# Optimization experiments

Measured on AMD Instinct MI355X. Metric: run time of the kernel, lower is better.

## Reference

```python
import jax, jax.numpy as jnp
import numpy as np

KERNEL = 3          # route_nms_kernel
MAX_ROUTES = 256    # max_routes (topk per image)
STRIDE = 4.0        # route_stride
MIN_SIZE = 32.0     # route_min_size
MAX_SIZE = 512.0    # route_max_size
POWER = 2.0         # route_score_power
B, H, W = 32, 512, 512


def setup_inputs() -> dict:
    key = jax.random.key(0)
    k1, k2, k3 = jax.random.split(key, 3)
    return {
        "route_logits": jax.random.normal(k1, (B, 1, H, W), dtype=jnp.float32),
        "scale_logits": jax.random.normal(k2, (B, 1, H, W), dtype=jnp.float32),
        "uncertainty_logits": jax.random.normal(k3, (B, 1, H, W), dtype=jnp.float32),
        "image_h": 2048,
        "image_w": 2048,
    }


def _local_max_pool(x):
    # x: [H, W]; 3x3 max pool, stride 1, pad kernel//2 (torch F.max_pool2d pads with -inf)
    pad = KERNEL // 2
    return jax.lax.reduce_window(x, -jnp.inf, jax.lax.max,
                                 (KERNEL, KERNEL), (1, 1),
                                 [(pad, pad), (pad, pad)])


def reference(route_logits, scale_logits, uncertainty_logits, image_h, image_w):
    # score_map = sigmoid(logits)^power * (1 - 0.35*sigmoid(uncertainty))  (use_route_uncertainty=True)
    score_map = jnp.power(jax.nn.sigmoid(route_logits), POWER)
    score_map = score_map * (1.0 - 0.35 * jax.nn.sigmoid(uncertainty_logits))
    img_h = jnp.float32(image_h)
    img_w = jnp.float32(image_w)
    width = route_logits.shape[-1]

    def per_image(batch_idx, scores2d, scale2d, unc2d):
        pooled = _local_max_pool(scores2d)
        filtered = jnp.where(scores2d == pooled, scores2d, -1.0)  # masked_fill(~mask, -1)
        values, indices = jax.lax.top_k(filtered.reshape(-1), MAX_ROUTES)
        valid = values > 0.0  # torch filters values>0; here kept as fixed-shape mask
        ys = indices // width
        xs = indices % width
        cx = (xs.astype(jnp.float32) + 0.5) * STRIDE
        cy = (ys.astype(jnp.float32) + 0.5) * STRIDE
        scale_g = scale2d[ys, xs]
        unc = jax.nn.sigmoid(unc2d[ys, xs])
        side = MIN_SIZE + jax.nn.sigmoid(scale_g) * (MAX_SIZE - MIN_SIZE)
        side = side * (1.0 + 0.25 * unc)
        half = side * 0.5
        x1 = jnp.clip(cx - half, 0.0, img_w - 1.0)
        y1 = jnp.clip(cy - half, 0.0, img_h - 1.0)
        x2 = jnp.clip(cx + half, 1.0, img_w)
        y2 = jnp.clip(cy + half, 1.0, img_h)
        rois = jnp.stack([jnp.full_like(x1, batch_idx), x1, y1, x2, y2], axis=1)  # [K,5]
        rois = jnp.where(valid[:, None], rois, 0.0)
        vals = jnp.where(valid, values, 0.0)
        return rois, vals, valid

    batch_ids = jnp.arange(route_logits.shape[0], dtype=jnp.float32)
    rois, scores, valid = jax.vmap(per_image)(
        batch_ids, score_map[:, 0], scale_logits[:, 0], uncertainty_logits[:, 0])
    # rois: [B, K, 5], scores: [B, K], valid: [B, K] (per_image_counts = valid.sum(-1))
    return rois, scores, valid
```

## Files before the change

kernel.cpp:

```cpp
#include <hip/hip_runtime.h>
#include <cstdint>
#include <cstddef>

#define BATCH 32
#define IMH 512
#define IMW 512
#define KMAX 256

#define RPW 4
#define NBLKX 2
#define NYG (IMH / RPW)
#define NL1 (NBLKX * NYG)
#define NM1 (NL1 / 4)
#define WCAP 256

typedef unsigned long long u64;

__device__ __forceinline__ float sigmoidf_(float x) {
    return 1.0f / (1.0f + expf(-x));
}
__device__ __forceinline__ float scoref_(float r, float u) {
    const float sg = sigmoidf_(r);
    return sg * sg * (1.0f - 0.35f * sigmoidf_(u));
}

#define SHF(v, jj, dm) do {                                         \
    const u64 o_ = __shfl_xor((v), (jj), 64);                       \
    const bool take_ = ((((lane & (jj)) == 0) == (dm)) == ((v) < o_)); \
    (v) = take_ ? o_ : (v);                                         \
} while (0)

#define RMAX(a, b) do {                                             \
    const u64 hi_ = ((a) > (b)) ? (a) : (b);                        \
    const u64 lo_ = ((a) > (b)) ? (b) : (a);                        \
    (a) = hi_; (b) = lo_;                                           \
} while (0)

#define RMIN(a, b) do {                                             \
    const u64 hi_ = ((a) > (b)) ? (a) : (b);                        \
    const u64 lo_ = ((a) > (b)) ? (b) : (a);                        \
    (a) = lo_; (b) = hi_;                                           \
} while (0)

__device__ __forceinline__ void clean256(u64& v0, u64& v1, u64& v2, u64& v3,
                                         const int lane) {
    RMAX(v0, v2); RMAX(v1, v3);
    RMAX(v0, v1); RMAX(v2, v3);
    #pragma unroll
    for (int j = 32; j > 0; j >>= 1) {
        SHF(v0, j, true); SHF(v1, j, true); SHF(v2, j, true); SHF(v3, j, true);
    }
}

__device__ __forceinline__ void sort256(u64& v0, u64& v1, u64& v2, u64& v3,
                                        const int lane) {
    #pragma unroll
    for (int k = 2; k <= 32; k <<= 1) {
        #pragma unroll
        for (int j = k >> 1; j > 0; j >>= 1) {
            const bool dm = ((lane & k) == 0);
            SHF(v0, j, dm); SHF(v1, j, dm); SHF(v2, j, dm); SHF(v3, j, dm);
        }
    }
    #pragma unroll
    for (int j = 32; j > 0; j >>= 1) {
        SHF(v0, j, true); SHF(v1, j, false); SHF(v2, j, true); SHF(v3, j, false);
    }
    RMAX(v0, v1); RMIN(v2, v3);
    #pragma unroll
    for (int j = 32; j > 0; j >>= 1) {
        SHF(v0, j, true); SHF(v1, j, true); SHF(v2, j, false); SHF(v3, j, false);
    }
    clean256(v0, v1, v2, v3, lane);
}

__device__ __forceinline__ void sort128(u64& v0, u64& v1, const int lane) {
    #pragma unroll
    for (int k = 2; k <= 32; k <<= 1) {
        #pragma unroll
        for (int j = k >> 1; j > 0; j >>= 1) {
            const bool dm = ((lane & k) == 0);
            SHF(v0, j, dm); SHF(v1, j, dm);
        }
    }
    #pragma unroll
    for (int j = 32; j > 0; j >>= 1) {
        SHF(v0, j, true); SHF(v1, j, false);
    }
    RMAX(v0, v1);
    #pragma unroll
    for (int j = 32; j > 0; j >>= 1) {
        SHF(v0, j, true); SHF(v1, j, true);
    }
}

__device__ __forceinline__ void merge256(u64& v0, u64& v1, u64& v2, u64& v3,
                                         u64 w0, u64 w1, u64 w2, u64 w3,
                                         const int lane) {
    const int rl = 63 ^ lane;
    const u64 b0 = __shfl(w3, rl, 64);
    const u64 b1 = __shfl(w2, rl, 64);
    const u64 b2 = __shfl(w1, rl, 64);
    const u64 b3 = __shfl(w0, rl, 64);
    v0 = (v0 > b0) ? v0 : b0;
    v1 = (v1 > b1) ? v1 : b1;
    v2 = (v2 > b2) ? v2 : b2;
    v3 = (v3 > b3) ? v3 : b3;
    clean256(v0, v1, v2, v3, lane);
}

__device__ __forceinline__ void load256(const u64* p, u64& v0, u64& v1,
                                        u64& v2, u64& v3, const int lane) {
    v0 = p[lane]; v1 = p[lane + 64]; v2 = p[lane + 128]; v3 = p[lane + 192];
}
__device__ __forceinline__ void store256(u64* p, u64 v0, u64 v1,
                                         u64 v2, u64 v3, const int lane) {
    p[lane] = v0; p[lane + 64] = v1; p[lane + 128] = v2; p[lane + 192] = v3;
}

__device__ __forceinline__ void merge4s(const u64* p,
                                        u64& a0, u64& a1, u64& a2, u64& a3,
                                        const int lane) {
    load256(p, a0, a1, a2, a3, lane);
    u64 w0, w1, w2, w3;
    load256(p + KMAX, w0, w1, w2, w3, lane);
    merge256(a0, a1, a2, a3, w0, w1, w2, w3, lane);
    u64 c0, c1, c2, c3;
    load256(p + 2 * KMAX, c0, c1, c2, c3, lane);
    load256(p + 3 * KMAX, w0, w1, w2, w3, lane);
    merge256(c0, c1, c2, c3, w0, w1, w2, w3, lane);
    merge256(a0, a1, a2, a3, c0, c1, c2, c3, lane);
}

__global__ __launch_bounds__(128)
void score_nms_kernel(const float* __restrict__ route,
                      const float* __restrict__ unc,
                      u64* __restrict__ top) {
    const int b    = blockIdx.z;
    const int w    = threadIdx.x >> 6;
    const int lane = threadIdx.x & 63;
    const int yg   = blockIdx.y * 2 + w;
    const int y0   = yg * RPW;
    const int x0   = blockIdx.x * 256 + lane * 4;
    const int list = yg * NBLKX + blockIdx.x;

    __shared__ u64 lcand[2 * WCAP];
    u64* myR = lcand + w * WCAP;

    const float* rB = route + (size_t)b * IMH * IMW;
    const float* uB = unc   + (size_t)b * IMH * IMW;

    int ex = -1;
    if (lane == 0)       ex = x0 - 1;
    else if (lane == 63) ex = x0 + 4;
    const bool eAct = (ex >= 0 && ex < IMW);

    const u64 laneMaskLt = (1ull << lane) - 1ull;
    int wcnt = 0;

    float sP[4], hP1[4], hP2[4];
    #pragma unroll
    for (int j = 0; j < 4; ++j) { sP[j] = -INFINITY; hP1[j] = -INFINITY; hP2[j] = -INFINITY; }

    const int ylast = y0 + RPW;
    bool v = (y0 - 1 >= 0);
    float4 r4, u4; float er = 0.f, eu = 0.f;
    if (v) {
        r4 = *(const float4*)(rB + (size_t)(y0 - 1) * IMW + x0);
        u4 = *(const float4*)(uB + (size_t)(y0 - 1) * IMW + x0);
        if (eAct) { er = rB[(size_t)(y0 - 1) * IMW + ex]; eu = uB[(size_t)(y0 - 1) * IMW + ex]; }
    }

    for (int y = y0 - 1; y <= ylast; ++y) {
        const int yn = y + 1;
        const bool vn = (yn <= ylast) && (yn < IMH);
        float4 r4n, u4n; float ern = 0.f, eun = 0.f;
        if (vn) {
            r4n = *(const float4*)(rB + (size_t)yn * IMW + x0);
            u4n = *(const float4*)(uB + (size_t)yn * IMW + x0);
            if (eAct) { ern = rB[(size_t)yn * IMW + ex]; eun = uB[(size_t)yn * IMW + ex]; }
        }

        float sC[4], hmC[4];
        float es = -INFINITY;
        if (v && eAct) es = scoref_(er, eu);
        if (v) {
            sC[0] = scoref_(r4.x, u4.x);
            sC[1] = scoref_(r4.y, u4.y);
            sC[2] = scoref_(r4.z, u4.z);
            sC[3] = scoref_(r4.w, u4.w);
        } else {
            sC[0] = sC[1] = sC[2] = sC[3] = -INFINITY;
        }
        float lft = __shfl_up(sC[3], 1, 64);
        if (lane == 0) lft = es;
        float rgt = __shfl_down(sC[0], 1, 64);
        if (lane == 63) rgt = es;
        if (v) {
            hmC[0] = fmaxf(fmaxf(lft,   sC[0]), sC[1]);
            hmC[1] = fmaxf(fmaxf(sC[0], sC[1]), sC[2]);
            hmC[2] = fmaxf(fmaxf(sC[1], sC[2]), sC[3]);
            hmC[3] = fmaxf(fmaxf(sC[2], sC[3]), rgt);
        } else {
            hmC[0] = hmC[1] = hmC[2] = hmC[3] = -INFINITY;
        }

        if (y >= y0 + 1) {
            const int yo = y - 1;
            bool p[4]; int cntT = 0;
            #pragma unroll
            for (int j = 0; j < 4; ++j) {
                const float m9 = fmaxf(fmaxf(hP2[j], hP1[j]), hmC[j]);
                p[j] = (sP[j] >= m9);
                cntT += p[j] ? 1 : 0;
            }
            const u64 B0 = __ballot(cntT & 1);
            const u64 B1 = __ballot(cntT & 2);
            const u64 B2 = __ballot(cntT & 4);
            const int total = __popcll(B0) + 2 * __popcll(B1) + 4 * __popcll(B2);
            if (total > 0) {
                const int prefix = __popcll(B0 & laneMaskLt) + 2 * __popcll(B1 & laneMaskLt)
                                 + 4 * __popcll(B2 & laneMaskLt);
                int mb = wcnt + prefix;
                #pragma unroll
                for (int j = 0; j < 4; ++j) {
                    if (p[j]) {
                        const unsigned idx = (unsigned)(yo * IMW + (x0 + j));
                        const u64 key = ((u64)__float_as_uint(sP[j]) << 32) | (unsigned)(~idx);
                        if (mb < WCAP) myR[mb] = key;
                        ++mb;
                    }
                }
                wcnt += total;
            }
        }

        #pragma unroll
        for (int j = 0; j < 4; ++j) { hP2[j] = hP1[j]; hP1[j] = hmC[j]; sP[j] = sC[j]; }
        r4 = r4n; u4 = u4n; er = ern; eu = eun; v = vn;
    }

    const int m = (wcnt < WCAP) ? wcnt : WCAP;
    u64 a0, a1, a2, a3;
    if (m <= 128) {
        a0 = (lane      < m) ? myR[lane]      : 0ull;
        a1 = (lane + 64 < m) ? myR[lane + 64] : 0ull;
        sort128(a0, a1, lane);
        a2 = 0ull; a3 = 0ull;
    } else {
        a0 = (lane       < m) ? myR[lane]       : 0ull;
        a1 = (lane + 64  < m) ? myR[lane + 64]  : 0ull;
        a2 = (lane + 128 < m) ? myR[lane + 128] : 0ull;
        a3 = (lane + 192 < m) ? myR[lane + 192] : 0ull;
        sort256(a0, a1, a2, a3, lane);
    }

    u64* seg = top + ((size_t)b * NL1 + list) * KMAX;
    store256(seg, a0, a1, a2, a3, lane);
}

__global__ __launch_bounds__(128)
void merge4_kernel(const u64* __restrict__ in, int nin,
                   u64* __restrict__ out_) {
    const int w    = threadIdx.x >> 6;
    const int lane = threadIdx.x & 63;
    const int o    = blockIdx.x * 2 + w;
    const int b    = blockIdx.y;
    const int nout = nin / 4;
    if (o >= nout) return;

    const u64* L = in + ((size_t)b * nin + o * 4) * KMAX;
    u64 a0, a1, a2, a3;
    merge4s(L, a0, a1, a2, a3, lane);

    u64* out = out_ + ((size_t)b * nout + o) * KMAX;
    store256(out, a0, a1, a2, a3, lane);
}

__global__ __launch_bounds__(1024)
void fused_tail_kernel(const u64* __restrict__ mid,
                       const float* __restrict__ scale,
                       const float* __restrict__ unc,
                       const int* __restrict__ imh,
                       const int* __restrict__ imw,
                       float* __restrict__ rois,
                       float* __restrict__ scoresOut,
                       float* __restrict__ validOut) {
    const int b    = blockIdx.x;
    const int tid  = threadIdx.x;
    const int w    = tid >> 6;
    const int lane = tid & 63;

    __shared__ u64 bufA[16 * KMAX];
    __shared__ u64 bufB[8 * KMAX];

    {
        const u64* G = mid + ((size_t)b * NM1 + 4 * w) * KMAX;
        u64 a0, a1, a2, a3;
        merge4s(G, a0, a1, a2, a3, lane);
        store256(bufA + (size_t)w * KMAX, a0, a1, a2, a3, lane);
    }
    __syncthreads();

    u64* src = bufA;
    u64* dst = bufB;
    int nl = 16;
    while (nl > 1) {
        const int half = nl >> 1;
        const int E = half * KMAX;
        for (int p = tid; p < E; p += 1024) {
            const int h = p >> 8;
            const int i = p & (KMAX - 1);
            const u64 a = src[(2 * h) * KMAX + i];
            const u64 c = src[(2 * h + 1) * KMAX + (KMAX - 1 - i)];
            dst[p] = (a > c) ? a : c;
        }
        __syncthreads();
        for (int j = KMAX >> 1; j > 0; j >>= 1) {
            for (int p = tid; p < (E >> 1); p += 1024) {
                const int i   = ((p & ~(j - 1)) << 1) | (p & (j - 1));
                const int ixj = i | j;
                const u64 a = dst[i];
                const u64 c = dst[ixj];
                if (a < c) { dst[i] = c; dst[ixj] = a; }
            }
            __syncthreads();
        }
        u64* t = src; src = dst; dst = t;
        nl = half;
    }

    if (tid < KMAX) {
        const u64 k = src[tid];
        const float value = __uint_as_float((unsigned)(k >> 32));
        const bool valid  = (k != 0ull) && (value > 0.0f);

        float r0 = 0.f, r1 = 0.f, r2 = 0.f, r3 = 0.f, r4 = 0.f, sv = 0.f, vv = 0.f;
        if (valid) {
            const unsigned idx = ~(unsigned)(k & 0xFFFFFFFFull);
            const int y = (int)(idx / IMW);
            const int x = (int)(idx % IMW);
            const float cx = ((float)x + 0.5f) * 4.0f;
            const float cy = ((float)y + 0.5f) * 4.0f;
            const float sg = scale[(size_t)b * IMH * IMW + idx];
            const float uu = unc[(size_t)b * IMH * IMW + idx];
            const float su = sigmoidf_(uu);
            float side = 32.0f + sigmoidf_(sg) * (512.0f - 32.0f);
            side = side * (1.0f + 0.25f * su);
            const float half2 = side * 0.5f;
            const float fw = (float)imw[0];
            const float fh = (float)imh[0];
            r0 = (float)b;
            r1 = fminf(fmaxf(cx - half2, 0.0f), fw - 1.0f);
            r2 = fminf(fmaxf(cy - half2, 0.0f), fh - 1.0f);
            r3 = fminf(fmaxf(cx + half2, 1.0f), fw);
            r4 = fminf(fmaxf(cy + half2, 1.0f), fh);
            sv = value;
            vv = 1.0f;
        }
        float* roiP = rois + ((size_t)b * KMAX + tid) * 5;
        roiP[0] = r0; roiP[1] = r1; roiP[2] = r2; roiP[3] = r3; roiP[4] = r4;
        scoresOut[b * KMAX + tid] = sv;
        validOut[b * KMAX + tid]  = vv;
    }
}

extern "C" void kernel_launch(void* const* d_in, const int* in_sizes, int n_in,
                              void* d_out, int out_size, void* d_ws, size_t ws_size,
                              hipStream_t stream) {
    const float* route = (const float*)d_in[0];
    const float* scale = (const float*)d_in[1];
    const float* unc   = (const float*)d_in[2];
    const int*   imh   = (const int*)d_in[3];
    const int*   imw   = (const int*)d_in[4];

    u64* top  = (u64*)d_ws;
    u64* mid1 = top + (size_t)BATCH * NL1 * KMAX;

    float* rois      = (float*)d_out;
    float* scoresOut = rois + (size_t)BATCH * KMAX * 5;
    float* validOut  = scoresOut + (size_t)BATCH * KMAX;

    dim3 grid1(NBLKX, NYG / 2, BATCH);
    score_nms_kernel<<<grid1, 128, 0, stream>>>(route, unc, top);

    dim3 grid2(NM1 / 2, BATCH);
    merge4_kernel<<<grid2, 128, 0, stream>>>(top, NL1, mid1);

    fused_tail_kernel<<<BATCH, 1024, 0, stream>>>(mid1, scale, unc, imh, imw,
                                                  rois, scoresOut, validOut);
}
```

Measured before the change: 62.72 us.

## Split score computation into separate pass and add extra merge stage before tail

Score computation moves out of the NMS kernel into a standalone elementwise kernel that writes a score map to workspace, which the NMS kernel then reads. This avoids recomputing sigmoids for halo rows and edge pixels and halves the loads per pixel inside the NMS kernel. The fused tail's first merge level becomes a separate merge4 launch, and the tail runs on 512 threads using a plain copy into shared memory. In exchange, a 32 MB score map is written and read back through global memory and two extra kernel launches are added.

```diff
diff --git a/kernel.cpp b/kernel.cpp
--- a/kernel.cpp
+++ b/kernel.cpp
@@ -12,7 +12,10 @@
 #define NYG (IMH / RPW)
 #define NL1 (NBLKX * NYG)
 #define NM1 (NL1 / 4)
+#define NMID (NM1 / 4)
 #define WCAP 256
+
+#define TPB2 512
 
 typedef unsigned long long u64;
 
@@ -132,9 +135,23 @@
     merge256(a0, a1, a2, a3, c0, c1, c2, c3, lane);
 }
 
+__global__ __launch_bounds__(256)
+void score_map_kernel(const float* __restrict__ route,
+                      const float* __restrict__ unc,
+                      float* __restrict__ smap) {
+    const size_t i = ((size_t)blockIdx.x * 256 + threadIdx.x) * 4;
+    const float4 r4 = *(const float4*)(route + i);
+    const float4 u4 = *(const float4*)(unc + i);
+    float4 s4;
+    s4.x = scoref_(r4.x, u4.x);
+    s4.y = scoref_(r4.y, u4.y);
+    s4.z = scoref_(r4.z, u4.z);
+    s4.w = scoref_(r4.w, u4.w);
+    *(float4*)(smap + i) = s4;
+}
+
 __global__ __launch_bounds__(128)
-void score_nms_kernel(const float* __restrict__ route,
-                      const float* __restrict__ unc,
+void score_nms_kernel(const float* __restrict__ smap,
                       u64* __restrict__ top) {
     const int b    = blockIdx.z;
     const int w    = threadIdx.x >> 6;
@@ -147,8 +164,7 @@
     __shared__ u64 lcand[2 * WCAP];
     u64* myR = lcand + w * WCAP;
 
-    const float* rB = route + (size_t)b * IMH * IMW;
-    const float* uB = unc   + (size_t)b * IMH * IMW;
+    const float* sB = smap + (size_t)b * IMH * IMW;
 
     int ex = -1;
     if (lane == 0)       ex = x0 - 1;
@@ -164,38 +180,33 @@
 
     const int ylast = y0 + RPW;
     bool v = (y0 - 1 >= 0);
-    float4 r4, u4; float er = 0.f, eu = 0.f;
+    float4 s4; float es = -INFINITY;
     if (v) {
-        r4 = *(const float4*)(rB + (size_t)(y0 - 1) * IMW + x0);
-        u4 = *(const float4*)(uB + (size_t)(y0 - 1) * IMW + x0);
-        if (eAct) { er = rB[(size_t)(y0 - 1) * IMW + ex]; eu = uB[(size_t)(y0 - 1) * IMW + ex]; }
+        s4 = *(const float4*)(sB + (size_t)(y0 - 1) * IMW + x0);
+        if (eAct) es = sB[(size_t)(y0 - 1) * IMW + ex];
     }
 
     for (int y = y0 - 1; y <= ylast; ++y) {
         const int yn = y + 1;
         const bool vn = (yn <= ylast) && (yn < IMH);
-        float4 r4n, u4n; float ern = 0.f, eun = 0.f;
+        float4 s4n; float esn = -INFINITY;
         if (vn) {
-            r4n = *(const float4*)(rB + (size_t)yn * IMW + x0);
-            u4n = *(const float4*)(uB + (size_t)yn * IMW + x0);
-            if (eAct) { ern = rB[(size_t)yn * IMW + ex]; eun = uB[(size_t)yn * IMW + ex]; }
+            s4n = *(const float4*)(sB + (size_t)yn * IMW + x0);
+            if (eAct) esn = sB[(size_t)yn * IMW + ex];
         }
 
         float sC[4], hmC[4];
-        float es = -INFINITY;
-        if (v && eAct) es = scoref_(er, eu);
+        float ecur = -INFINITY;
+        if (v && eAct) ecur = es;
         if (v) {
-            sC[0] = scoref_(r4.x, u4.x);
-            sC[1] = scoref_(r4.y, u4.y);
-            sC[2] = scoref_(r4.z, u4.z);
-            sC[3] = scoref_(r4.w, u4.w);
+            sC[0] = s4.x; sC[1] = s4.y; sC[2] = s4.z; sC[3] = s4.w;
         } else {
             sC[0] = sC[1] = sC[2] = sC[3] = -INFINITY;
         }
         float lft = __shfl_up(sC[3], 1, 64);
-        if (lane == 0) lft = es;
+        if (lane == 0) lft = ecur;
         float rgt = __shfl_down(sC[0], 1, 64);
-        if (lane == 63) rgt = es;
+        if (lane == 63) rgt = ecur;
         if (v) {
             hmC[0] = fmaxf(fmaxf(lft,   sC[0]), sC[1]);
             hmC[1] = fmaxf(fmaxf(sC[0], sC[1]), sC[2]);
@@ -237,7 +248,7 @@
 
         #pragma unroll
         for (int j = 0; j < 4; ++j) { hP2[j] = hP1[j]; hP1[j] = hmC[j]; sP[j] = sC[j]; }
-        r4 = r4n; u4 = u4n; er = ern; eu = eun; v = vn;
+        s4 = s4n; es = esn; v = vn;
     }
 
     const int m = (wcnt < WCAP) ? wcnt : WCAP;
@@ -277,38 +288,32 @@
     store256(out, a0, a1, a2, a3, lane);
 }
 
-__global__ __launch_bounds__(1024)
-void fused_tail_kernel(const u64* __restrict__ mid,
-                       const float* __restrict__ scale,
-                       const float* __restrict__ unc,
-                       const int* __restrict__ imh,
-                       const int* __restrict__ imw,
-                       float* __restrict__ rois,
-                       float* __restrict__ scoresOut,
-                       float* __restrict__ validOut) {
-    const int b    = blockIdx.x;
-    const int tid  = threadIdx.x;
-    const int w    = tid >> 6;
-    const int lane = tid & 63;
-
-    __shared__ u64 bufA[16 * KMAX];
-    __shared__ u64 bufB[8 * KMAX];
-
-    {
-        const u64* G = mid + ((size_t)b * NM1 + 4 * w) * KMAX;
-        u64 a0, a1, a2, a3;
-        merge4s(G, a0, a1, a2, a3, lane);
-        store256(bufA + (size_t)w * KMAX, a0, a1, a2, a3, lane);
-    }
+__global__ __launch_bounds__(TPB2)
+void tail_kernel(const u64* __restrict__ mid,
+                 const float* __restrict__ scale,
+                 const float* __restrict__ unc,
+                 const int* __restrict__ imh,
+                 const int* __restrict__ imw,
+                 float* __restrict__ rois,
+                 float* __restrict__ scoresOut,
+                 float* __restrict__ validOut) {
+    const int b   = blockIdx.x;
+    const int tid = threadIdx.x;
+
+    __shared__ u64 bufA[NMID * KMAX];
+    __shared__ u64 bufB[(NMID / 2) * KMAX];
+
+    const u64* tb = mid + (size_t)b * NMID * KMAX;
+    for (int i = tid; i < NMID * KMAX; i += TPB2) bufA[i] = tb[i];
     __syncthreads();
 
     u64* src = bufA;
     u64* dst = bufB;
-    int nl = 16;
+    int nl = NMID;
     while (nl > 1) {
         const int half = nl >> 1;
         const int E = half * KMAX;
-        for (int p = tid; p < E; p += 1024) {
+        for (int p = tid; p < E; p += TPB2) {
             const int h = p >> 8;
             const int i = p & (KMAX - 1);
             const u64 a = src[(2 * h) * KMAX + i];
@@ -317,7 +322,7 @@
         }
         __syncthreads();
         for (int j = KMAX >> 1; j > 0; j >>= 1) {
-            for (int p = tid; p < (E >> 1); p += 1024) {
+            for (int p = tid; p < (E >> 1); p += TPB2) {
                 const int i   = ((p & ~(j - 1)) << 1) | (p & (j - 1));
                 const int ixj = i | j;
                 const u64 a = dst[i];
@@ -374,19 +379,27 @@
     const int*   imh   = (const int*)d_in[3];
     const int*   imw   = (const int*)d_in[4];
 
-    u64* top  = (u64*)d_ws;
-    u64* mid1 = top + (size_t)BATCH * NL1 * KMAX;
+    float* smap = (float*)d_ws;
+    u64*   top  = (u64*)((char*)d_ws + (size_t)BATCH * IMH * IMW * sizeof(float));
+    u64*   mid1 = top  + (size_t)BATCH * NL1 * KMAX;
+    u64*   mid2 = mid1 + (size_t)BATCH * NM1 * KMAX;
 
     float* rois      = (float*)d_out;
     float* scoresOut = rois + (size_t)BATCH * KMAX * 5;
     float* validOut  = scoresOut + (size_t)BATCH * KMAX;
 
+    const int n4 = BATCH * IMH * IMW / 4;
+    score_map_kernel<<<n4 / 256, 256, 0, stream>>>(route, unc, smap);
+
     dim3 grid1(NBLKX, NYG / 2, BATCH);
-    score_nms_kernel<<<grid1, 128, 0, stream>>>(route, unc, top);
+    score_nms_kernel<<<grid1, 128, 0, stream>>>(smap, top);
 
     dim3 grid2(NM1 / 2, BATCH);
     merge4_kernel<<<grid2, 128, 0, stream>>>(top, NL1, mid1);
 
-    fused_tail_kernel<<<BATCH, 1024, 0, stream>>>(mid1, scale, unc, imh, imw,
-                                                  rois, scoresOut, validOut);
-}
+    dim3 grid3(NMID / 2, BATCH);
+    merge4_kernel<<<grid3, 128, 0, stream>>>(mid1, NM1, mid2);
+
+    tail_kernel<<<BATCH, TPB2, 0, stream>>>(mid2, scale, unc,
+                                            imh, imw, rois, scoresOut, validOut);
+}
```

New measurement: 63.53 us. Within noise of the previous version (+1.3%).
